# Performance work log

Measured on AMD Instinct MI355X. Metric: run time of the kernel, lower is better.

Reference implementation:

```python
import jax, jax.numpy as jnp
import numpy as np

B, T, D, U = 64, 512, 1024, 1024


def hard_sigmoid(x):
    # keras hard_sigmoid: clip(0.2*x + 0.5, 0, 1)
    return jnp.clip(0.2 * x + 0.5, 0.0, 1.0)


def setup_inputs() -> dict:
    key = jax.random.key(0)
    ks = jax.random.split(key, 6)
    x = jax.random.normal(ks[0], (B, T, D), jnp.float32)
    # glorot-ish scaled params
    kernel = jax.random.normal(ks[1], (D, 4 * U), jnp.float32) * (1.0 / np.sqrt(D).astype(np.float32))
    recurrent_kernel = jax.random.normal(ks[2], (U, 4 * U), jnp.float32) * (1.0 / np.sqrt(U).astype(np.float32))
    peephole_kernel = jax.random.normal(ks[3], (U, 3 * U), jnp.float32) * (1.0 / np.sqrt(U).astype(np.float32))
    projection_kernel = jax.random.normal(ks[4], (U, U), jnp.float32) * (1.0 / np.sqrt(U).astype(np.float32))
    # unit_forget_bias: [zeros(U), ones(U), zeros(2U)] for (i, f, c, o)
    bias = jnp.concatenate([jnp.zeros((U,), jnp.float32), jnp.ones((U,), jnp.float32), jnp.zeros((2 * U,), jnp.float32)])
    h0 = jnp.zeros((B, U), jnp.float32)
    c0 = jnp.zeros((B, U), jnp.float32)
    return {"x": x, "h0": h0, "c0": c0, "kernel": kernel, "recurrent_kernel": recurrent_kernel,
            "peephole_kernel": peephole_kernel, "projection_kernel": projection_kernel, "bias": bias}


def reference(x, h0, c0, kernel, recurrent_kernel, peephole_kernel, projection_kernel, bias):
    U_ = h0.shape[-1]
    Pi = peephole_kernel[:, :U_]
    Pf = peephole_kernel[:, U_:2 * U_]
    Po = peephole_kernel[:, 2 * U_:3 * U_]

    def step(carry, x_t):
        h, c = carry
        # fused gate pre-activations: [B, 4U]
        z = x_t @ kernel + h @ recurrent_kernel + bias
        zi, zf, zc, zo = jnp.split(z, 4, axis=-1)
        i = hard_sigmoid(zi + c @ Pi)            # input gate w/ peephole on c_{t-1}
        f = hard_sigmoid(zf + c @ Pf)            # forget gate w/ peephole on c_{t-1}
        c_new = f * c + i * jnp.tanh(zc)
        o = hard_sigmoid(zo + c_new @ Po)        # output gate w/ peephole on c_t
        # residual LSTM: project tanh(c_t), add residual input, gate by o
        h_new = o * (jnp.tanh(c_new) @ projection_kernel + x_t)
        return (h_new, c_new), h_new

    xs = jnp.swapaxes(x, 0, 1)  # [T, B, D]
    (_, _), hs = jax.lax.scan(step, (h0, c0), xs)
    return jnp.swapaxes(hs, 0, 1)  # [B, T, U]
```

## Files before the change

kernel.cpp:

```cpp
#include <hip/hip_runtime.h>
#include <cstdint>
#include <cstddef>

#define NB 64
#define NT 512
#define ND 1024
#define NU 1024

typedef short s16x8 __attribute__((ext_vector_type(8)));
typedef float f32x4 __attribute__((ext_vector_type(4)));
typedef unsigned int u32x2 __attribute__((ext_vector_type(2)));
typedef unsigned short u16;

__device__ __forceinline__ u16 f2bf(float f) {
  unsigned int u = __float_as_uint(f);
  u += 0x7fffu + ((u >> 16) & 1u);
  return (u16)(u >> 16);
}
__device__ __forceinline__ float bf2f(u16 s) {
  return __uint_as_float(((unsigned int)s) << 16);
}
__device__ __forceinline__ float hsig(float x) {
  return fminf(fmaxf(0.2f * x + 0.5f, 0.0f), 1.0f);
}
__device__ __forceinline__ f32x4 mfma16(s16x8 a, s16x8 b, f32x4 c) {
  return __builtin_amdgcn_mfma_f32_16x16x32_bf16(a, b, c, 0, 0, 0);
}

__device__ __forceinline__ void atomic_swap_u32(unsigned int* p, unsigned int v) {
  asm volatile("global_atomic_swap %0, %1, off" :: "v"(p), "v"(v) : "memory");
}

template <int STAGED>
__device__ __forceinline__ void ldx4(s16x8& d, const u16* a) {
  if constexpr (STAGED)
    asm volatile("global_load_dwordx4 %0, %1, off" : "=v"(d) : "v"(a));
  else
    asm volatile("global_load_dwordx4 %0, %1, off sc0 sc1" : "=v"(d) : "v"(a));
}

#define WAIT_VM0() do { \
    asm volatile("s_waitcnt vmcnt(0)" ::: "memory"); \
    __builtin_amdgcn_sched_barrier(0); \
  } while (0)

__global__ __launch_bounds__(256) void xw_gemm(const float* __restrict__ X,
                                               const float* __restrict__ W,
                                               u16* __restrict__ XW) {
  __shared__ u16 Al[128][72];
  __shared__ u16 Bl[128][72];
  const int tid = threadIdx.x;
  const int lane = tid & 63;
  const int wv = tid >> 6;
  const int m0 = (blockIdx.x >> 5) * 128;
  const int n0 = (blockIdx.x & 31) * 128;
  f32x4 acc[4][4];
#pragma unroll
  for (int i = 0; i < 4; ++i)
#pragma unroll
    for (int j = 0; j < 4; ++j) acc[i][j] = (f32x4){0.f, 0.f, 0.f, 0.f};

  for (int kt = 0; kt < 1024; kt += 64) {
    {
      const int r = tid >> 1, hh = (tid & 1) * 32;
      const float* src = X + (size_t)(m0 + r) * 1024 + kt + hh;
      u16* dst = &Al[r][hh];
#pragma unroll
      for (int j = 0; j < 8; ++j) {
        float4 v = ((const float4*)src)[j];
        dst[j * 4 + 0] = f2bf(v.x); dst[j * 4 + 1] = f2bf(v.y);
        dst[j * 4 + 2] = f2bf(v.z); dst[j * 4 + 3] = f2bf(v.w);
      }
    }
    {
      const int kr = tid >> 2, q = (tid & 3) * 32;
      const float* src = W + (size_t)(kt + kr) * 4096 + n0 + q;
#pragma unroll
      for (int j = 0; j < 8; ++j) {
        float4 v = ((const float4*)src)[j];
        const int n = q + j * 4;
        Bl[n + 0][kr] = f2bf(v.x); Bl[n + 1][kr] = f2bf(v.y);
        Bl[n + 2][kr] = f2bf(v.z); Bl[n + 3][kr] = f2bf(v.w);
      }
    }
    __syncthreads();
    const int wm = (wv >> 1) * 64, wn = (wv & 1) * 64;
    const int row = lane & 15, kq = (lane >> 4) * 8;
#pragma unroll
    for (int ks = 0; ks < 2; ++ks) {
      s16x8 af[4], bq[4];
#pragma unroll
      for (int i = 0; i < 4; ++i) af[i] = *(const s16x8*)&Al[wm + i * 16 + row][ks * 32 + kq];
#pragma unroll
      for (int j = 0; j < 4; ++j) bq[j] = *(const s16x8*)&Bl[wn + j * 16 + row][ks * 32 + kq];
#pragma unroll
      for (int i = 0; i < 4; ++i)
#pragma unroll
        for (int j = 0; j < 4; ++j) acc[i][j] = mfma16(af[i], bq[j], acc[i][j]);
    }
    __syncthreads();
  }
  const int wm = (wv >> 1) * 64, wn = (wv & 1) * 64;
  const int col16 = lane & 15, rq = (lane >> 4) * 4;
#pragma unroll
  for (int i = 0; i < 4; ++i)
#pragma unroll
    for (int j = 0; j < 4; ++j)
#pragma unroll
      for (int q = 0; q < 4; ++q) {
        const int m = m0 + wm + i * 16 + rq + q;
        const int n = n0 + wn + j * 16 + col16;
        const int t = m & 511, b = m >> 9;
        const int g = n >> 10, uu = n & 1023;
        const int ugrp = uu >> 3, ul2 = uu & 7;
        XW[(((size_t)ugrp * 512 + t) * 64 + b) * 32 + ul2 * 4 + g] = f2bf(acc[i][j][q]);
      }
}

__global__ void init_comm(const float* __restrict__ h0, const float* __restrict__ c0,
                          u16* hini, u16* cini) {
  const int i = blockIdx.x * 256 + threadIdx.x;
  hini[i] = f2bf(h0[i]);
  cini[i] = f2bf(c0[i]);
}

__device__ __forceinline__ void gbar(unsigned int* flags, int bid, int tid, unsigned int ep) {
  __syncthreads();
  if (tid == 0) atomic_swap_u32(flags + bid * 16, ep);
  unsigned int* f = flags + ((((tid & 127) << 1) | (bid & 1)) * 16);
  for (;;) {
    unsigned int v;
    asm volatile("global_load_dword %0, %1, off sc0 sc1\n\ts_waitcnt vmcnt(0)"
                 : "=v"(v) : "v"(f) : "memory");
    if (v >= ep) break;
    __builtin_amdgcn_s_sleep(1);
  }
  __syncthreads();
}

#define WLDS_B   (64 * 1032 * 2)
#define ZOFF     WLDS_B
#define POFF     (ZOFF + 32 * 33 * 4)
#define OOFF     (POFF + 32 * 17 * 4)
#define SMEM_B   (OOFF + 32 * 17 * 4)
#define STEP_E   65536

template <int STAGED>
__global__ __launch_bounds__(256, 1) void lstm_loop(
    const float* __restrict__ rec, const float* __restrict__ peep,
    const float* __restrict__ projw, const float* __restrict__ bias,
    const float* __restrict__ x, const u16* __restrict__ xw,
    float* __restrict__ out,
    u16* hini, u16* cini, u16* thsg,
    u16* hst, u16* cst, u16* thst,
    unsigned int* flags, const float* __restrict__ c0) {
  extern __shared__ char smem[];
  u16 (*wlds)[1032] = (u16(*)[1032])smem;
  float (*zlds)[33] = (float(*)[33])(smem + ZOFF);
  float (*plds)[17] = (float(*)[17])(smem + POFF);
  float (*olds)[17] = (float(*)[17])(smem + OOFF);

  const int tid = threadIdx.x;
  const int lane = tid & 63;
  const int wv = tid >> 6;
  const int bid = blockIdx.x;
  const int ugrp = bid >> 1;
  const int row0 = (bid & 1) * 32;
  const int u0 = ugrp * 8;

  for (int g = 0; g < 8; ++g) {
    const int c = g * 8 + (tid & 3) * 2;
    const float* sp; int stride, scol;
    if (c < 32)      { sp = rec;   stride = 4096; scol = (c >> 3) * 1024 + u0 + (c & 7); }
    else if (c < 48) { sp = peep;  stride = 3072; scol = ((c - 32) >> 3) * 1024 + u0 + (c & 7); }
    else if (c < 56) { sp = peep;  stride = 3072; scol = 2048 + u0 + (c & 7); }
    else             { sp = projw; stride = 1024; scol = u0 + (c - 56); }
#pragma unroll 4
    for (int p = 0; p < 16; ++p) {
      const int k = p * 64 + (tid >> 2);
      float2 v = *(const float2*)(sp + (size_t)k * stride + scol);
      wlds[c][k] = f2bf(v.x);
      wlds[c + 1][k] = f2bf(v.y);
    }
  }

  const int r = tid >> 3;
  const int ul = tid & 7;
  const int brow = row0 + r;
  const int u = u0 + ul;
  const float b_i = bias[u], b_f = bias[1024 + u], b_c = bias[2048 + u], b_o = bias[3072 + u];
  float cst0 = c0[brow * 1024 + u];
  float cstv = cst0;

  const int fcol = lane & 15;
  const int kofs = (lane >> 4) * 8;

  s16x8 av[32];
  u32x2 xwp;
  float xp;

  {
    const u16* xr0 = xw + (((size_t)ugrp * 512 + 0) * 64 + brow) * 32 + ul * 4;
    asm volatile("global_load_dwordx2 %0, %1, off" : "=v"(xwp) : "v"(xr0));
    const float* xs0 = x + (size_t)brow * (512 * 1024) + u;
    asm volatile("global_load_dword %0, %1, off" : "=v"(xp) : "v"(xs0));
  }
  if (wv < 2) {
    const u16* ap = cini + (size_t)(row0 + wv * 16 + fcol) * 1024 + kofs;
#pragma unroll
    for (int kt = 0; kt < 32; ++kt)
      asm volatile("global_load_dwordx4 %0, %1, off sc0 sc1"
                   : "=v"(av[kt]) : "v"(ap + kt * 32));
  }
  WAIT_VM0();
  __syncthreads();

  for (int t = 0; t < NT; ++t) {
    float zo_reg, xres, hv;
    const size_t xo = (size_t)brow * (512 * 1024) + (size_t)t * 1024 + u;

    const u16* hsrc; u16* cpub; u16* thpub; const u16* csrc; const u16* thsrc; u16* hpub;
    if constexpr (STAGED) {
      hsrc  = t ? (hst + (size_t)(t - 1) * STEP_E) : hini;
      hpub  = hst + (size_t)t * STEP_E;
      cpub  = cst + (size_t)t * STEP_E;   csrc  = cpub;
      thpub = thst + (size_t)t * STEP_E;  thsrc = thpub;
    } else {
      hsrc = hini; hpub = hini; cpub = cini; csrc = cini; thpub = thsg; thsrc = thsg;
    }

    if (wv >= 2) {
      const int rt = wv - 2;
      const u16* ap = hsrc + (size_t)(row0 + rt * 16 + fcol) * 1024 + kofs;
#pragma unroll
      for (int kt = 0; kt < 32; ++kt) ldx4<STAGED>(av[kt], ap + kt * 32);
      WAIT_VM0();
      f32x4 accA = {0.f, 0.f, 0.f, 0.f}, accB = {0.f, 0.f, 0.f, 0.f};
      const u16* bp0 = &wlds[fcol][kofs];
      const u16* bp1 = &wlds[16 + fcol][kofs];
#pragma unroll
      for (int kt = 0; kt < 32; ++kt) {
        accA = mfma16(av[kt], *(const s16x8*)(bp0 + kt * 32), accA);
        accB = mfma16(av[kt], *(const s16x8*)(bp1 + kt * 32), accB);
      }
      const int srow = rt * 16 + (lane >> 4) * 4;
#pragma unroll
      for (int q = 0; q < 4; ++q) {
        zlds[srow + q][fcol] = accA[q];
        zlds[srow + q][16 + fcol] = accB[q];
      }
    } else {
      f32x4 accP = {0.f, 0.f, 0.f, 0.f};
      const u16* bp = &wlds[32 + fcol][kofs];
#pragma unroll
      for (int kt = 0; kt < 32; ++kt)
        accP = mfma16(av[kt], *(const s16x8*)(bp + kt * 32), accP);
      const int srow = wv * 16 + (lane >> 4) * 4;
#pragma unroll
      for (int q = 0; q < 4; ++q) plds[srow + q][fcol] = accP[q];
    }
    __syncthreads();
    {
      const float xw_i = bf2f((u16)(xwp[0] & 0xffffu));
      const float xw_f = bf2f((u16)(xwp[0] >> 16));
      const float xw_c = bf2f((u16)(xwp[1] & 0xffffu));
      const float xw_o = bf2f((u16)(xwp[1] >> 16));
      xres = xp;
      const float zi = zlds[r][ul]      + xw_i + b_i + plds[r][ul];
      const float zf = zlds[r][8 + ul]  + xw_f + b_f + plds[r][8 + ul];
      const float zc = zlds[r][16 + ul] + xw_c + b_c;
      zo_reg         = zlds[r][24 + ul] + xw_o + b_o;
      const float ig = hsig(zi), fg = hsig(zf);
      cstv = fg * cstv + ig * tanhf(zc);
      const float th = tanhf(cstv);
      const unsigned int cb = f2bf(cstv), tb = f2bf(th);
      const unsigned int cpart = (unsigned int)__shfl_xor((int)cb, 1);
      const unsigned int tpart = (unsigned int)__shfl_xor((int)tb, 1);
      if ((ul & 1) == 0) {
        atomic_swap_u32((unsigned int*)(cpub + brow * 1024 + u), (cpart << 16) | cb);
        atomic_swap_u32((unsigned int*)(thpub + brow * 1024 + u), (tpart << 16) | tb);
      }
    }
    WAIT_VM0();
    gbar(flags, bid, tid, 2 * t + 1);

    {
      const int prt = wv & 1;
      const u16* ap = ((wv < 2) ? csrc : thsrc)
                      + (size_t)(row0 + prt * 16 + fcol) * 1024 + kofs;
#pragma unroll
      for (int kt = 0; kt < 32; ++kt) ldx4<STAGED>(av[kt], ap + kt * 32);
      {
        const int tn = (t + 1 < NT) ? (t + 1) : t;
        const u16* xrn = xw + (((size_t)ugrp * 512 + tn) * 64 + brow) * 32 + ul * 4;
        asm volatile("global_load_dwordx2 %0, %1, off" : "=v"(xwp) : "v"(xrn));
        const float* xsn = x + (size_t)brow * (512 * 1024) + (size_t)tn * 1024 + u;
        asm volatile("global_load_dword %0, %1, off" : "=v"(xp) : "v"(xsn));
      }
      asm volatile("s_waitcnt vmcnt(2)" ::: "memory");
      __builtin_amdgcn_sched_barrier(0);
      f32x4 acc = {0.f, 0.f, 0.f, 0.f};
      const u16* bp = &wlds[48 + fcol][kofs];
#pragma unroll
      for (int kt = 0; kt < 32; ++kt)
        acc = mfma16(av[kt], *(const s16x8*)(bp + kt * 32), acc);
      const int srow = prt * 16 + (lane >> 4) * 4;
      if (wv < 2) {
        if (fcol < 8) {
#pragma unroll
          for (int q = 0; q < 4; ++q) olds[srow + q][fcol] = acc[q];
        }
      } else {
        if (fcol >= 8) {
#pragma unroll
          for (int q = 0; q < 4; ++q) olds[srow + q][fcol] = acc[q];
        }
      }
    }
    __syncthreads();
    {
      const float og = hsig(zo_reg + olds[r][ul]);
      const float pv = olds[r][8 + ul] + xres;
      hv = og * pv;
      const unsigned int hb = f2bf(hv);
      const unsigned int hpart = (unsigned int)__shfl_xor((int)hb, 1);
      if ((ul & 1) == 0)
        atomic_swap_u32((unsigned int*)(hpub + brow * 1024 + u), (hpart << 16) | hb);
    }
    WAIT_VM0();
    gbar(flags, bid, tid, 2 * t + 2);
    asm volatile("global_store_dword %0, %1, off" :: "v"(out + xo), "v"(hv) : "memory");
  }
}

extern "C" void kernel_launch(void* const* d_in, const int* in_sizes, int n_in,
                              void* d_out, int out_size, void* d_ws, size_t ws_size,
                              hipStream_t stream) {
  const float* x    = (const float*)d_in[0];
  const float* h0   = (const float*)d_in[1];
  const float* c0   = (const float*)d_in[2];
  const float* W    = (const float*)d_in[3];
  const float* R    = (const float*)d_in[4];
  const float* P    = (const float*)d_in[5];
  const float* PRJ  = (const float*)d_in[6];
  const float* bias = (const float*)d_in[7];
  float* out = (float*)d_out;
  char* ws = (char*)d_ws;

  const size_t XW_BYTES = (size_t)32768 * 4096 * 2;
  size_t off = XW_BYTES;
  u16* xw   = (u16*)ws;
  u16* hini = (u16*)(ws + off); off += 131072;
  u16* cini = (u16*)(ws + off); off += 131072;
  u16* thsg = (u16*)(ws + off); off += 131072;
  unsigned int* flags = (unsigned int*)(ws + off); off += 16384;
  const size_t base_need = off;
  u16* hst = (u16*)(ws + off); off += (size_t)NT * 131072;
  u16* cst = (u16*)(ws + off); off += (size_t)NT * 131072;
  u16* thst = (u16*)(ws + off); off += (size_t)NT * 131072;
  const size_t staged_need = off;
  if (ws_size < base_need) return;
  const int staged = (ws_size >= staged_need) ? 1 : 0;

  (void)hipFuncSetAttribute(reinterpret_cast<const void*>(&lstm_loop<1>),
                            hipFuncAttributeMaxDynamicSharedMemorySize, 160 * 1024);
  (void)hipFuncSetAttribute(reinterpret_cast<const void*>(&lstm_loop<0>),
                            hipFuncAttributeMaxDynamicSharedMemorySize, 160 * 1024);

  hipMemsetAsync(flags, 0, 16384, stream);
  hipLaunchKernelGGL(init_comm, dim3(256), dim3(256), 0, stream, h0, c0, hini, cini);
  hipLaunchKernelGGL(xw_gemm, dim3(8192), dim3(256), 0, stream, x, W, xw);

  void* args[15];
  args[0] = (void*)&R;     args[1] = (void*)&P;     args[2] = (void*)&PRJ;
  args[3] = (void*)&bias;  args[4] = (void*)&x;     args[5] = (void*)&xw;
  args[6] = (void*)&out;   args[7] = (void*)&hini;  args[8] = (void*)&cini;
  args[9] = (void*)&thsg;  args[10] = (void*)&hst;  args[11] = (void*)&cst;
  args[12] = (void*)&thst; args[13] = (void*)&flags; args[14] = (void*)&c0;

  const void* fn = staged ? (const void*)&lstm_loop<1> : (const void*)&lstm_loop<0>;
  hipError_t e = hipLaunchCooperativeKernel(fn, dim3(256), dim3(256),
                                            args, (unsigned int)SMEM_B, stream);
  if (e != hipSuccess) {
    if (staged)
      hipLaunchKernelGGL((lstm_loop<1>), dim3(256), dim3(256), SMEM_B, stream,
                         R, P, PRJ, bias, x, xw, out, hini, cini, thsg,
                         hst, cst, thst, flags, c0);
    else
      hipLaunchKernelGGL((lstm_loop<0>), dim3(256), dim3(256), SMEM_B, stream,
                         R, P, PRJ, bias, x, xw, out, hini, cini, thsg,
                         hst, cst, thst, flags, c0);
  }
}
```

Before: 7.389 ms.

## Pretranspose W to bf16, vectorize LDS staging, widen publish atomics, fast tanh

Adds a pre-pass that converts the input kernel W to bf16 and transposes it, so the XW GEMM can stage B tiles with vector copies instead of scattered per-element fp32 conversion stores. It also packs the X tile conversion into 16-byte LDS stores. Inside the recurrent loop, tanhf is replaced by an exp-based tanh, and the h/c/tanh(c) publish uses 64-bit atomic swaps from one lane in four instead of 32-bit swaps from one in two. The z buffer pitch is changed. The trade-offs are an extra workspace buffer and kernel launch, plus a less accurate tanh.

Result: faster. 7.035 ms (-4.8%).

```diff
diff --git a/kernel.cpp b/kernel.cpp
--- a/kernel.cpp
+++ b/kernel.cpp
@@ -10,6 +10,7 @@
 typedef short s16x8 __attribute__((ext_vector_type(8)));
 typedef float f32x4 __attribute__((ext_vector_type(4)));
 typedef unsigned int u32x2 __attribute__((ext_vector_type(2)));
+typedef unsigned int u32x4 __attribute__((ext_vector_type(4)));
 typedef unsigned short u16;
 
 __device__ __forceinline__ u16 f2bf(float f) {
@@ -23,12 +24,19 @@
 __device__ __forceinline__ float hsig(float x) {
   return fminf(fmaxf(0.2f * x + 0.5f, 0.0f), 1.0f);
 }
+__device__ __forceinline__ float ftanh(float x) {
+  float e = __expf(2.0f * x);
+  return 1.0f - 2.0f / (e + 1.0f);
+}
 __device__ __forceinline__ f32x4 mfma16(s16x8 a, s16x8 b, f32x4 c) {
   return __builtin_amdgcn_mfma_f32_16x16x32_bf16(a, b, c, 0, 0, 0);
 }
 
 __device__ __forceinline__ void atomic_swap_u32(unsigned int* p, unsigned int v) {
   asm volatile("global_atomic_swap %0, %1, off" :: "v"(p), "v"(v) : "memory");
+}
+__device__ __forceinline__ void atomic_swap_u64(unsigned int* p, u32x2 v) {
+  asm volatile("global_atomic_swap_x2 %0, %1, off" :: "v"(p), "v"(v) : "memory");
 }
 
 template <int STAGED>
@@ -44,8 +52,37 @@
     __builtin_amdgcn_sched_barrier(0); \
   } while (0)
 
+__global__ __launch_bounds__(256) void wt_cvt(const float* __restrict__ W,
+                                              u16* __restrict__ Wt) {
+  __shared__ u16 T[64][65];
+  const int tid = threadIdx.x;
+  const int k0 = (blockIdx.x & 15) * 64;
+  const int n0 = (blockIdx.x >> 4) * 64;
+  const int r = tid >> 2, c4 = (tid & 3) * 16;
+  {
+    const float* src = W + (size_t)(k0 + r) * 4096 + n0 + c4;
+#pragma unroll
+    for (int j = 0; j < 4; ++j) {
+      float4 v = ((const float4*)src)[j];
+      T[r][c4 + j * 4 + 0] = f2bf(v.x); T[r][c4 + j * 4 + 1] = f2bf(v.y);
+      T[r][c4 + j * 4 + 2] = f2bf(v.z); T[r][c4 + j * 4 + 3] = f2bf(v.w);
+    }
+  }
+  __syncthreads();
+  {
+    u16 tmp[16];
+#pragma unroll
+    for (int i = 0; i < 16; ++i) tmp[i] = T[c4 + i][r];
+    u16* dst = Wt + (size_t)(n0 + r) * 1024 + k0 + c4;
+    *(s16x8*)dst = *(s16x8*)tmp;
+    *(s16x8*)(dst + 8) = *(s16x8*)(tmp + 8);
+  }
+}
+
+template <int WT>
 __global__ __launch_bounds__(256) void xw_gemm(const float* __restrict__ X,
                                                const float* __restrict__ W,
+                                               const u16* __restrict__ Wt,
                                                u16* __restrict__ XW) {
   __shared__ u16 Al[128][72];
   __shared__ u16 Bl[128][72];
@@ -65,14 +102,35 @@
       const int r = tid >> 1, hh = (tid & 1) * 32;
       const float* src = X + (size_t)(m0 + r) * 1024 + kt + hh;
       u16* dst = &Al[r][hh];
-#pragma unroll
-      for (int j = 0; j < 8; ++j) {
-        float4 v = ((const float4*)src)[j];
-        dst[j * 4 + 0] = f2bf(v.x); dst[j * 4 + 1] = f2bf(v.y);
-        dst[j * 4 + 2] = f2bf(v.z); dst[j * 4 + 3] = f2bf(v.w);
-      }
-    }
-    {
+      if constexpr (WT) {
+#pragma unroll
+        for (int j = 0; j < 4; ++j) {
+          float4 v0 = ((const float4*)src)[2 * j];
+          float4 v1 = ((const float4*)src)[2 * j + 1];
+          u32x4 q;
+          q[0] = ((unsigned)f2bf(v0.y) << 16) | f2bf(v0.x);
+          q[1] = ((unsigned)f2bf(v0.w) << 16) | f2bf(v0.z);
+          q[2] = ((unsigned)f2bf(v1.y) << 16) | f2bf(v1.x);
+          q[3] = ((unsigned)f2bf(v1.w) << 16) | f2bf(v1.z);
+          *(u32x4*)(dst + j * 8) = q;
+        }
+      } else {
+#pragma unroll
+        for (int j = 0; j < 8; ++j) {
+          float4 v = ((const float4*)src)[j];
+          dst[j * 4 + 0] = f2bf(v.x); dst[j * 4 + 1] = f2bf(v.y);
+          dst[j * 4 + 2] = f2bf(v.z); dst[j * 4 + 3] = f2bf(v.w);
+        }
+      }
+    }
+    if constexpr (WT) {
+      const int n = tid >> 1, kh = (tid & 1) * 32;
+      const u16* src = Wt + (size_t)(n0 + n) * 1024 + kt + kh;
+      u16* dst = &Bl[n][kh];
+#pragma unroll
+      for (int j = 0; j < 4; ++j)
+        *(s16x8*)(dst + j * 8) = *(const s16x8*)(src + j * 8);
+    } else {
       const int kr = tid >> 2, q = (tid & 3) * 32;
       const float* src = W + (size_t)(kt + kr) * 4096 + n0 + q;
 #pragma unroll
@@ -140,7 +198,7 @@
 
 #define WLDS_B   (64 * 1032 * 2)
 #define ZOFF     WLDS_B
-#define POFF     (ZOFF + 32 * 33 * 4)
+#define POFF     (ZOFF + 32 * 34 * 4)
 #define OOFF     (POFF + 32 * 17 * 4)
 #define SMEM_B   (OOFF + 32 * 17 * 4)
 #define STEP_E   65536
@@ -156,7 +214,7 @@
     unsigned int* flags, const float* __restrict__ c0) {
   extern __shared__ char smem[];
   u16 (*wlds)[1032] = (u16(*)[1032])smem;
-  float (*zlds)[33] = (float(*)[33])(smem + ZOFF);
+  float (*zlds)[34] = (float(*)[34])(smem + ZOFF);
   float (*plds)[17] = (float(*)[17])(smem + POFF);
   float (*olds)[17] = (float(*)[17])(smem + OOFF);
 
@@ -189,8 +247,7 @@
   const int brow = row0 + r;
   const int u = u0 + ul;
   const float b_i = bias[u], b_f = bias[1024 + u], b_c = bias[2048 + u], b_o = bias[3072 + u];
-  float cst0 = c0[brow * 1024 + u];
-  float cstv = cst0;
+  float cstv = c0[brow * 1024 + u];
 
   const int fcol = lane & 15;
   const int kofs = (lane >> 4) * 8;
@@ -271,14 +328,18 @@
       const float zc = zlds[r][16 + ul] + xw_c + b_c;
       zo_reg         = zlds[r][24 + ul] + xw_o + b_o;
       const float ig = hsig(zi), fg = hsig(zf);
-      cstv = fg * cstv + ig * tanhf(zc);
-      const float th = tanhf(cstv);
+      cstv = fg * cstv + ig * ftanh(zc);
+      const float th = ftanh(cstv);
       const unsigned int cb = f2bf(cstv), tb = f2bf(th);
-      const unsigned int cpart = (unsigned int)__shfl_xor((int)cb, 1);
-      const unsigned int tpart = (unsigned int)__shfl_xor((int)tb, 1);
-      if ((ul & 1) == 0) {
-        atomic_swap_u32((unsigned int*)(cpub + brow * 1024 + u), (cpart << 16) | cb);
-        atomic_swap_u32((unsigned int*)(thpub + brow * 1024 + u), (tpart << 16) | tb);
+      const unsigned int cp = ((unsigned)__shfl_xor((int)cb, 1) << 16) | cb;
+      const unsigned int tp = ((unsigned)__shfl_xor((int)tb, 1) << 16) | tb;
+      const unsigned int cp2 = (unsigned)__shfl_xor((int)cp, 2);
+      const unsigned int tp2 = (unsigned)__shfl_xor((int)tp, 2);
+      if ((ul & 3) == 0) {
+        u32x2 cq; cq[0] = cp; cq[1] = cp2;
+        u32x2 tq; tq[0] = tp; tq[1] = tp2;
+        atomic_swap_u64((unsigned int*)(cpub + brow * 1024 + u), cq);
+        atomic_swap_u64((unsigned int*)(thpub + brow * 1024 + u), tq);
       }
     }
     WAIT_VM0();
@@ -323,9 +384,12 @@
       const float pv = olds[r][8 + ul] + xres;
       hv = og * pv;
       const unsigned int hb = f2bf(hv);
-      const unsigned int hpart = (unsigned int)__shfl_xor((int)hb, 1);
-      if ((ul & 1) == 0)
-        atomic_swap_u32((unsigned int*)(hpub + brow * 1024 + u), (hpart << 16) | hb);
+      const unsigned int hp = ((unsigned)__shfl_xor((int)hb, 1) << 16) | hb;
+      const unsigned int hp2 = (unsigned)__shfl_xor((int)hp, 2);
+      if ((ul & 3) == 0) {
+        u32x2 hq; hq[0] = hp; hq[1] = hp2;
+        atomic_swap_u64((unsigned int*)(hpub + brow * 1024 + u), hq);
+      }
     }
     WAIT_VM0();
     gbar(flags, bid, tid, 2 * t + 2);
@@ -359,8 +423,11 @@
   u16* cst = (u16*)(ws + off); off += (size_t)NT * 131072;
   u16* thst = (u16*)(ws + off); off += (size_t)NT * 131072;
   const size_t staged_need = off;
+  u16* Wt = (u16*)(ws + off); off += (size_t)4096 * 1024 * 2;
+  const size_t wt_need = off;
   if (ws_size < base_need) return;
   const int staged = (ws_size >= staged_need) ? 1 : 0;
+  const int wt = (ws_size >= wt_need) ? 1 : 0;
 
   (void)hipFuncSetAttribute(reinterpret_cast<const void*>(&lstm_loop<1>),
                             hipFuncAttributeMaxDynamicSharedMemorySize, 160 * 1024);
@@ -369,7 +436,12 @@
 
   hipMemsetAsync(flags, 0, 16384, stream);
   hipLaunchKernelGGL(init_comm, dim3(256), dim3(256), 0, stream, h0, c0, hini, cini);
-  hipLaunchKernelGGL(xw_gemm, dim3(8192), dim3(256), 0, stream, x, W, xw);
+  if (wt) {
+    hipLaunchKernelGGL(wt_cvt, dim3(1024), dim3(256), 0, stream, W, Wt);
+    hipLaunchKernelGGL((xw_gemm<1>), dim3(8192), dim3(256), 0, stream, x, W, Wt, xw);
+  } else {
+    hipLaunchKernelGGL((xw_gemm<0>), dim3(8192), dim3(256), 0, stream, x, W, Wt, xw);
+  }
 
   void* args[15];
   args[0] = (void*)&R;     args[1] = (void*)&P;     args[2] = (void*)&PRJ;
```
